# Kernel optimization log

Hardware: AMD Instinct MI355X
Metric: run time of the kernel (lower is better)

The kernel has to match this reference:

```python
import jax, jax.numpy as jnp
import numpy as np

B, S, E = 2, 2048, 1024
H = 32
DK = E // H  # 32, must equal H for the bilinear einsum to type-check
FFN = 4096
EPS = 1e-5


def layer_norm(x, g, b):
    m = jnp.mean(x, axis=-1, keepdims=True)
    v = jnp.mean((x - m) ** 2, axis=-1, keepdims=True)
    return (x - m) * jax.lax.rsqrt(v + EPS) * g + b


def setup_inputs() -> dict:
    key = jax.random.key(0)
    ks = jax.random.split(key, 16)
    sc = lambda fan_in: 1.0 / np.sqrt(fan_in)
    return {
        "x": jax.random.normal(ks[0], (B, S, E), jnp.float32),
        "Wq": jax.random.normal(ks[1], (E, E), jnp.float32) * sc(E),
        "bq": jax.random.normal(ks[2], (E,), jnp.float32) * 0.02,
        "Wk": jax.random.normal(ks[3], (E, E), jnp.float32) * sc(E),
        "bk": jax.random.normal(ks[4], (E,), jnp.float32) * 0.02,
        "Wv": jax.random.normal(ks[5], (E, E), jnp.float32) * sc(E),
        "bv": jax.random.normal(ks[6], (E,), jnp.float32) * 0.02,
        "kernelW": jax.random.normal(ks[7], (DK, H), jnp.float32),
        "Wo": jax.random.normal(ks[8], (E, E), jnp.float32) * sc(E),
        "bo": jax.random.normal(ks[9], (E,), jnp.float32) * 0.02,
        "W1": jax.random.normal(ks[10], (E, FFN), jnp.float32) * sc(E),
        "b1": jax.random.normal(ks[11], (FFN,), jnp.float32) * 0.02,
        "W2": jax.random.normal(ks[12], (FFN, E), jnp.float32) * sc(FFN),
        "b2": jax.random.normal(ks[13], (E,), jnp.float32) * 0.02,
        "g1": jnp.ones((E,), jnp.float32),
        "beta1": jnp.zeros((E,), jnp.float32),
        "g2": jnp.ones((E,), jnp.float32),
        "beta2": jnp.zeros((E,), jnp.float32),
    }


def reference(x, Wq, bq, Wk, bk, Wv, bv, kernelW, Wo, bo, W1, b1, W2, b2, g1, beta1, g2, beta2):
    # projections -> [B, H, S, DK]
    split = lambda t: t.reshape(B, S, H, DK).transpose(0, 2, 1, 3)
    q = split(x @ Wq + bq)
    k = split(x @ Wk + bk)
    v = split(x @ Wv + bv)
    # bilinear quantum-kernel score: sim[b,h,i,j] = sum_d q[b,h,i,d]*W[d,h]*k[b,h,j,d]
    sim = jnp.einsum('bhqd,dh,bhkd->bhqk', q, kernelW, k)
    attn = jax.nn.softmax(sim, axis=-1)  # dropout is identity at eval
    out = jnp.matmul(attn, v)  # [B, H, S, DK]
    out = out.transpose(0, 2, 1, 3).reshape(B, S, E) @ Wo + bo
    x = layer_norm(x + out, g1, beta1)
    ffn = jax.nn.relu(x @ W1 + b1) @ W2 + b2
    return layer_norm(x + ffn, g2, beta2)
```

## Files before the change

### kernel.cpp

```cpp
#include <hip/hip_runtime.h>


typedef unsigned short u16;
typedef unsigned int u32;
typedef __bf16 bf16x8 __attribute__((ext_vector_type(8)));
typedef float f32x4 __attribute__((ext_vector_type(4)));
typedef float f32x16 __attribute__((ext_vector_type(16)));

__device__ __forceinline__ u16 f2b(float f) {
  union { float f; unsigned u; } x; x.f = f;
  unsigned r = x.u + 0x7FFFu + ((x.u >> 16) & 1u);
  return (u16)(r >> 16);
}

__device__ __forceinline__ float b2f(u16 u) {
  union { u32 u; float f; } x; x.u = (u32)u << 16; return x.f;
}

__device__ __forceinline__ unsigned pkbf(float lo, float hi) {
  unsigned r;
  asm("v_cvt_pk_bf16_f32 %0, %1, %2" : "=v"(r) : "v"(lo), "v"(hi));
  return r;
}

__device__ __forceinline__ float expo2(float x) {
#if __has_builtin(__builtin_amdgcn_exp2f)
  return __builtin_amdgcn_exp2f(x);
#else
  return exp2f(x);
#endif
}

#define GLDS16(gp, lp)                                                         \
  __builtin_amdgcn_global_load_lds(                                            \
      (const __attribute__((address_space(1))) void*)(gp),                     \
      (__attribute__((address_space(3))) void*)(lp), 16, 0, 0)

__global__ __launch_bounds__(256) void prep_kernel(
    const float* __restrict__ Wq, const float* __restrict__ Wk,
    const float* __restrict__ Wv, const float* __restrict__ Wo,
    const float* __restrict__ W1, const float* __restrict__ W2,
    const float* __restrict__ x, u16* __restrict__ WqT, u16* __restrict__ WoT,
    u16* __restrict__ W1T, u16* __restrict__ W2T, u16* __restrict__ xb) {
  __shared__ float tile[32][33];
  const int id = blockIdx.x;
  if (id < 12288) {
    const float* W; u16* WT; int K, N, bx, by;
    if (id < 4096) {
      const int w = id >> 10, local = id & 1023;
      bx = local & 31; by = local >> 5; K = 1024; N = 1024;
      W = (w == 0) ? Wq : (w == 1) ? Wk : (w == 2) ? Wv : Wo;
      WT = (w == 0) ? WqT : (w == 1) ? WqT + 1048576
           : (w == 2) ? WqT + 2097152 : WoT;
    } else if (id < 8192) {
      const int local = id - 4096;
      bx = local & 127; by = local >> 7; K = 1024; N = 4096;
      W = W1; WT = W1T;
    } else {
      const int local = id - 8192;
      bx = local & 31; by = local >> 5; K = 4096; N = 1024;
      W = W2; WT = W2T;
    }
    const int tx = threadIdx.x & 31, ty = threadIdx.x >> 5;
    const int n0 = bx * 32, k0 = by * 32;
#pragma unroll
    for (int i = 0; i < 4; ++i)
      tile[ty + 8 * i][tx] = W[(size_t)(k0 + ty + 8 * i) * N + n0 + tx];
    __syncthreads();
#pragma unroll
    for (int i = 0; i < 4; ++i)
      WT[(size_t)(n0 + ty + 8 * i) * K + k0 + tx] = f2b(tile[tx][ty + 8 * i]);
  } else {
    const int i = (id - 12288) * 256 + threadIdx.x;
    float4 v = ((const float4*)x)[i];
    ushort4 o;
    o.x = f2b(v.x); o.y = f2b(v.y); o.z = f2b(v.z); o.w = f2b(v.w);
    ((ushort4*)xb)[i] = o;
  }
}

template <int MODE, int BN>
__global__ __launch_bounds__(256) void gemmT(
    const u16* __restrict__ A, const u16* __restrict__ BT,
    const float* __restrict__ bias, const float* __restrict__ bias2,
    const float* __restrict__ bias3, const float* __restrict__ res,
    void* __restrict__ outp, const float* __restrict__ kW, int N_, int K_) {
  constexpr int ABYT = 128 * 32 * 2;
  constexpr int BBYT = BN * 32 * 2;
  constexpr int STRIDE = ABYT + BBYT;
  constexpr int MI = (BN == 128) ? 4 : 2;
  __shared__ __align__(16) char SH[2 * STRIDE];
  const int t = threadIdx.x, lane = t & 63, wid = t >> 6;
  const int gx = gridDim.x;
  const int id = blockIdx.y * gx + blockIdx.x;
  const int nb = gx * gridDim.y;
  const int sid = (id & 7) * (nb >> 3) + (id >> 3);
  const int bx = sid % gx;
  int by = sid / gx;
  int kh6 = 0;
  if constexpr (MODE == 6 || MODE == 7) { kh6 = by >> 5; by &= 31; }
  const int m0 = by * 128, n0 = bx * BN;
  const int wr = (BN == 128) ? (wid >> 1) * 64 : wid * 32;
  const int wc = (BN == 128) ? (wid & 1) * 64 : 0;
  const int lr = lane & 15, lg = lane >> 4;
  const int K = K_;
  const int koff = (MODE == 6) ? kh6 * 1024 : (MODE == 7) ? kh6 * 512 : 0;

  f32x4 acc[MI][4] = {};

  const u16* ga0 = A + (size_t)(m0 + (t >> 2)) * K + koff + (t & 3) * 8;
  const u16* ga1 = ga0 + (size_t)64 * K;
  const u16* gb0 = BT + (size_t)(n0 + (t >> 2)) * K + koff + (t & 3) * 8;
  const u16* gb1 = gb0 + (size_t)64 * K;
  const int stA = wid * 1024;

#define STAGE(CUR, KT)                                                         \
  {                                                                            \
    char* l_ = (char*)SH + (CUR) * STRIDE + stA;                               \
    const size_t o_ = (size_t)(KT) * 32;                                       \
    GLDS16(ga0 + o_, l_);                                                      \
    GLDS16(ga1 + o_, l_ + 4096);                                               \
    GLDS16(gb0 + o_, l_ + ABYT);                                               \
    if constexpr (BN == 128) GLDS16(gb1 + o_, l_ + ABYT + 4096);               \
  }

  const int nk = (MODE == 6) ? 32 : (MODE == 7) ? 16 : (K >> 5);
  STAGE(0, 0);
  __syncthreads();
  int cur = 0;
  for (int kt = 0; kt < nk; ++kt) {
    if (kt + 1 < nk) STAGE(cur ^ 1, kt + 1);
    const char* l = (const char*)SH + cur * STRIDE;
    bf16x8 af[MI], bf[4];
#pragma unroll
    for (int i = 0; i < MI; ++i)
      af[i] = *(const bf16x8*)(l + (wr + i * 16 + lr) * 64 + lg * 16);
#pragma unroll
    for (int i = 0; i < 4; ++i)
      bf[i] = *(const bf16x8*)(l + ABYT + (wc + i * 16 + lr) * 64 + lg * 16);
#pragma unroll
    for (int mi = 0; mi < MI; ++mi)
#pragma unroll
      for (int ni = 0; ni < 4; ++ni)
        acc[mi][ni] = __builtin_amdgcn_mfma_f32_16x16x32_bf16(
            af[mi], bf[ni], acc[mi][ni], 0, 0, 0);
    __syncthreads();
    cur ^= 1;
  }
#undef STAGE

#pragma unroll
  for (int mi = 0; mi < MI; ++mi) {
#pragma unroll
    for (int ni = 0; ni < 4; ++ni) {
      const int row = m0 + wr + mi * 16 + lg * 4;
      const int col = n0 + wc + ni * 16 + lr;
      f32x4 v = acc[mi][ni];
      if constexpr (MODE == 3) {
        const float bv = bias[col];
        u16* o = (u16*)outp;
#pragma unroll
        for (int r = 0; r < 4; ++r) {
          const int rr = row + r;
          float y = v[r] + bv;
          o[(size_t)rr * N_ + col] = f2b(y > 0.f ? y : 0.f);
        }
      } else if constexpr (MODE == 6) {
        u16* o = (kh6 < 2) ? ((u16*)outp + (size_t)kh6 * 4194304)
                           : ((u16*)res + (size_t)(kh6 - 2) * 4194304);
#pragma unroll
        for (int r = 0; r < 4; ++r) {
          const int rr = row + r;
          o[(size_t)rr * N_ + col] = f2b(v[r]);
        }
      } else if constexpr (MODE == 7) {
        u16* o = (kh6 == 0) ? (u16*)outp : (u16*)res;
#pragma unroll
        for (int r = 0; r < 4; ++r) {
          const int rr = row + r;
          o[(size_t)rr * N_ + col] = f2b(v[r]);
        }
      } else {
        const int proj = col >> 10, c = col & 1023;
        const int h = c >> 5, d = c & 31;
        u16* qout = (u16*)outp;
        if (proj == 0) {
          const float bv = bias[c];
          const float sc = kW[d * 32 + h] * 1.44269504089f;
#pragma unroll
          for (int r = 0; r < 4; ++r) {
            const int rr = row + r;
            const int bb = rr >> 11, s = rr & 2047;
            qout[(size_t)(((bb * 32 + h) * 2048) + s) * 32 + d] =
                f2b((v[r] + bv) * sc);
          }
        } else if (proj == 1) {
          const float bv = bias2[c];
          u16* kout = qout + 4194304;
          const int c2 = d >> 3;
#pragma unroll
          for (int r = 0; r < 4; ++r) {
            const int rr = row + r;
            const int bb = rr >> 11, s = rr & 2047;
            const int k = s & 63;
            const int g = ((k >> 5) << 1) | (c2 >> 1);
            kout[(size_t)(bb * 32 + h) * 65536 + (s >> 6) * 2048 + g * 512 +
                 (c2 & 1) * 256 + (k & 31) * 8 + (d & 7)] = f2b(v[r] + bv);
          }
        } else {
          const float bv = bias3[c];
          u16* vout = qout + 8388608;
          const int bb = row >> 11, s0 = row & 2047;
          const int k = s0 & 63;
          const int cc = k >> 3, rb = cc >> 1, hb = cc & 1, e = k & 7;
          ushort4 st;
          st.x = f2b(v[0] + bv); st.y = f2b(v[1] + bv);
          st.z = f2b(v[2] + bv); st.w = f2b(v[3] + bv);
          *(ushort4*)(vout + (size_t)(bb * 32 + h) * 65536 +
                      (s0 >> 6) * 2048 + rb * 512 + hb * 256 + d * 8 + e) = st;
        }
      }
    }
  }
}

__device__ __forceinline__ void attn_tile(
    const bf16x8& k0, const bf16x8& k1, const bf16x8& k2, const bf16x8& k3,
    const bf16x8& v0, const bf16x8& v1, const bf16x8& v2, const bf16x8& v3,
    const bf16x8& qb0, const bf16x8& qb1,
    f32x16& acc, float& la, float& lb, float& lc, float& ld) {
  const f32x16 z16 = {};
  f32x16 s0 = __builtin_amdgcn_mfma_f32_32x32x16_bf16(k0, qb0, z16, 0, 0, 0);
  s0 = __builtin_amdgcn_mfma_f32_32x32x16_bf16(k1, qb1, s0, 0, 0, 0);
  f32x16 s1 = __builtin_amdgcn_mfma_f32_32x32x16_bf16(k2, qb0, z16, 0, 0, 0);
  s1 = __builtin_amdgcn_mfma_f32_32x32x16_bf16(k3, qb1, s1, 0, 0, 0);
  float p0[16], p1[16];
#pragma unroll
  for (int r = 0; r < 16; ++r) p0[r] = expo2(s0[r]);
#pragma unroll
  for (int r = 0; r < 16; ++r) p1[r] = expo2(s1[r]);
#pragma unroll
  for (int r = 0; r < 4; ++r) {
    la += p0[r] + p1[r];
    lb += p0[4 + r] + p1[4 + r];
    lc += p0[8 + r] + p1[8 + r];
    ld += p0[12 + r] + p1[12 + r];
  }
  {
    u32 x0 = pkbf(p0[0], p0[1]), x1 = pkbf(p0[2], p0[3]);
    u32 y0 = pkbf(p0[4], p0[5]), y1 = pkbf(p0[6], p0[7]);
    asm("v_permlane32_swap_b32 %0, %1" : "+v"(x0), "+v"(y0));
    asm("v_permlane32_swap_b32 %0, %1" : "+v"(x1), "+v"(y1));
    union { u32 d[4]; bf16x8 v; } u;
    u.d[0] = x0; u.d[1] = x1; u.d[2] = y0; u.d[3] = y1;
    acc = __builtin_amdgcn_mfma_f32_32x32x16_bf16(v0, u.v, acc, 0, 0, 0);
  }
  {
    u32 x0 = pkbf(p0[8], p0[9]), x1 = pkbf(p0[10], p0[11]);
    u32 y0 = pkbf(p0[12], p0[13]), y1 = pkbf(p0[14], p0[15]);
    asm("v_permlane32_swap_b32 %0, %1" : "+v"(x0), "+v"(y0));
    asm("v_permlane32_swap_b32 %0, %1" : "+v"(x1), "+v"(y1));
    union { u32 d[4]; bf16x8 v; } u;
    u.d[0] = x0; u.d[1] = x1; u.d[2] = y0; u.d[3] = y1;
    acc = __builtin_amdgcn_mfma_f32_32x32x16_bf16(v1, u.v, acc, 0, 0, 0);
  }
  {
    u32 x0 = pkbf(p1[0], p1[1]), x1 = pkbf(p1[2], p1[3]);
    u32 y0 = pkbf(p1[4], p1[5]), y1 = pkbf(p1[6], p1[7]);
    asm("v_permlane32_swap_b32 %0, %1" : "+v"(x0), "+v"(y0));
    asm("v_permlane32_swap_b32 %0, %1" : "+v"(x1), "+v"(y1));
    union { u32 d[4]; bf16x8 v; } u;
    u.d[0] = x0; u.d[1] = x1; u.d[2] = y0; u.d[3] = y1;
    acc = __builtin_amdgcn_mfma_f32_32x32x16_bf16(v2, u.v, acc, 0, 0, 0);
  }
  {
    u32 x0 = pkbf(p1[8], p1[9]), x1 = pkbf(p1[10], p1[11]);
    u32 y0 = pkbf(p1[12], p1[13]), y1 = pkbf(p1[14], p1[15]);
    asm("v_permlane32_swap_b32 %0, %1" : "+v"(x0), "+v"(y0));
    asm("v_permlane32_swap_b32 %0, %1" : "+v"(x1), "+v"(y1));
    union { u32 d[4]; bf16x8 v; } u;
    u.d[0] = x0; u.d[1] = x1; u.d[2] = y0; u.d[3] = y1;
    acc = __builtin_amdgcn_mfma_f32_32x32x16_bf16(v3, u.v, acc, 0, 0, 0);
  }
}

__global__ __launch_bounds__(512) void attn_kernel(
    const u16* __restrict__ Q, const u16* __restrict__ K,
    const u16* __restrict__ VT, u16* __restrict__ O) {
  __shared__ __align__(16) char LDSB[32768];
  const int t = threadIdx.x, wid = t >> 6, lane = t & 63;
  const int qg = wid & 3, kh = wid >> 2;
  const int bid = blockIdx.x;
  const int swz = (bid & 7) * 128 + (bid >> 3);
  const int bh = swz >> 4;
  const int qt = swz & 15;
  const int q0 = qt * 128 + qg * 32;
  const int lq = lane & 31, hi = lane >> 5;
  const u16* Qh = Q + (size_t)bh * 65536;
  const u16* Kh = K + (size_t)bh * 65536;
  const u16* Vh = VT + (size_t)bh * 65536;

  const bf16x8 qb0 = *(const bf16x8*)(Qh + (size_t)(q0 + lq) * 32 + hi * 8);
  const bf16x8 qb1 = *(const bf16x8*)(Qh + (size_t)(q0 + lq) * 32 + 16 + hi * 8);

  const u16* kg = Kh + wid * 512 + lane * 8;
  const u16* vg = Vh + wid * 512 + lane * 8;
  const int lds_w = wid * 1024;

#define STAGEA(CUR, I)                                                         \
  if (wid < 4) {                                                               \
    char* b_ = LDSB + (CUR) * 16384 + lds_w;                                   \
    GLDS16(kg + (size_t)(I) * 2048, b_);                                       \
    GLDS16(vg + (size_t)(I) * 2048, b_ + 4096);                                \
    GLDS16(kg + (size_t)(16 + (I)) * 2048, b_ + 8192);                         \
    GLDS16(vg + (size_t)(16 + (I)) * 2048, b_ + 12288);                        \
  }

  f32x16 acc = {};
  float la = 0.f, lb = 0.f, lc = 0.f, ld = 0.f;

  STAGEA(0, 0);
  __syncthreads();
  int cur = 0;
#pragma unroll 1
  for (int i = 0; i < 16; ++i) {
    if (i < 15) STAGEA(cur ^ 1, i + 1);
    const char* kb = LDSB + cur * 16384 + kh * 8192 + lane * 16;
    const bf16x8 ka0 = *(const bf16x8*)(kb);
    const bf16x8 ka1 = *(const bf16x8*)(kb + 1024);
    const bf16x8 ka2 = *(const bf16x8*)(kb + 2048);
    const bf16x8 ka3 = *(const bf16x8*)(kb + 3072);
    const bf16x8 va0 = *(const bf16x8*)(kb + 4096);
    const bf16x8 va1 = *(const bf16x8*)(kb + 5120);
    const bf16x8 va2 = *(const bf16x8*)(kb + 6144);
    const bf16x8 va3 = *(const bf16x8*)(kb + 7168);
    attn_tile(ka0, ka1, ka2, ka3, va0, va1, va2, va3, qb0, qb1,
              acc, la, lb, lc, ld);
    __syncthreads();
    cur ^= 1;
  }
#undef STAGEA

  float lrun = (la + lb) + (lc + ld);
  lrun += __shfl_xor(lrun, 32);

  float* sm_acc = (float*)LDSB;
  float* sm_l = (float*)(LDSB + 16384);
  if (kh == 1) {
    sm_l[qg * 32 + lq] = lrun;
#pragma unroll
    for (int r = 0; r < 16; ++r) sm_acc[(qg * 64 + lane) * 16 + r] = acc[r];
  }
  __syncthreads();
  if (kh == 0) {
    const float inv = 1.f / (lrun + sm_l[qg * 32 + lq]);
    const int bb = bh >> 5, h = bh & 31;
    u16* o = O + (size_t)(bb * 2048 + q0 + lq) * 1024 + h * 32;
#pragma unroll
    for (int g = 0; g < 4; ++g) {
      ushort4 st;
      st.x = f2b((acc[g * 4 + 0] + sm_acc[(qg * 64 + lane) * 16 + g * 4 + 0]) * inv);
      st.y = f2b((acc[g * 4 + 1] + sm_acc[(qg * 64 + lane) * 16 + g * 4 + 1]) * inv);
      st.z = f2b((acc[g * 4 + 2] + sm_acc[(qg * 64 + lane) * 16 + g * 4 + 2]) * inv);
      st.w = f2b((acc[g * 4 + 3] + sm_acc[(qg * 64 + lane) * 16 + g * 4 + 3]) * inv);
      *(ushort4*)(o + g * 8 + hi * 4) = st;
    }
  }
}

__global__ __launch_bounds__(256) void ln1merge_kernel(
    const u16* __restrict__ P0, const u16* __restrict__ P1,
    const u16* __restrict__ R, const float* __restrict__ bias,
    const float* __restrict__ g, const float* __restrict__ b,
    u16* __restrict__ out) {
  const int wid = threadIdx.x >> 6, lane = threadIdx.x & 63;
  const int row = blockIdx.x * 4 + wid;
  const ushort4* A4 = (const ushort4*)(P0 + (size_t)row * 1024);
  const ushort4* B4 = (const ushort4*)(P1 + (size_t)row * 1024);
  const ushort4* R4 = (const ushort4*)(R + (size_t)row * 1024);
  const float4* Bi4 = (const float4*)bias;
  float4 xs[4];
  float s = 0.f, sq = 0.f;
#pragma unroll
  for (int i = 0; i < 4; ++i) {
    const int c = lane + i * 64;
    const ushort4 a = A4[c], pb = B4[c], rr = R4[c];
    const float4 bi = Bi4[c];
    float4 x;
    x.x = (b2f(a.x) + b2f(pb.x)) + b2f(rr.x) + bi.x;
    x.y = (b2f(a.y) + b2f(pb.y)) + b2f(rr.y) + bi.y;
    x.z = (b2f(a.z) + b2f(pb.z)) + b2f(rr.z) + bi.z;
    x.w = (b2f(a.w) + b2f(pb.w)) + b2f(rr.w) + bi.w;
    xs[i] = x;
    s += x.x + x.y + x.z + x.w;
    sq += x.x * x.x + x.y * x.y + x.z * x.z + x.w * x.w;
  }
#pragma unroll
  for (int m = 1; m < 64; m <<= 1) { s += __shfl_xor(s, m); sq += __shfl_xor(sq, m); }
  const float mean = s * (1.f / 1024.f);
  float var = sq * (1.f / 1024.f) - mean * mean;
  var = var > 0.f ? var : 0.f;
  const float rstd = rsqrtf(var + 1e-5f);
  const float4* g4 = (const float4*)g;
  const float4* b4 = (const float4*)b;
  ushort4* of = (ushort4*)(out + (size_t)row * 1024);
#pragma unroll
  for (int i = 0; i < 4; ++i) {
    const int c = lane + i * 64;
    const float4 gv = g4[c], bv = b4[c], x = xs[i];
    ushort4 yb;
    yb.x = f2b((x.x - mean) * rstd * gv.x + bv.x);
    yb.y = f2b((x.y - mean) * rstd * gv.y + bv.y);
    yb.z = f2b((x.z - mean) * rstd * gv.z + bv.z);
    yb.w = f2b((x.w - mean) * rstd * gv.w + bv.w);
    of[c] = yb;
  }
}

__global__ __launch_bounds__(256) void ln2sum_kernel(
    const u16* __restrict__ P0, const u16* __restrict__ P1,
    const u16* __restrict__ P2, const u16* __restrict__ P3,
    const u16* __restrict__ R, const float* __restrict__ bias,
    const float* __restrict__ g, const float* __restrict__ b,
    float* __restrict__ out) {
  const int wid = threadIdx.x >> 6, lane = threadIdx.x & 63;
  const int row = blockIdx.x * 4 + wid;
  const ushort4* A4 = (const ushort4*)(P0 + (size_t)row * 1024);
  const ushort4* B4 = (const ushort4*)(P1 + (size_t)row * 1024);
  const ushort4* C4 = (const ushort4*)(P2 + (size_t)row * 1024);
  const ushort4* D4 = (const ushort4*)(P3 + (size_t)row * 1024);
  const ushort4* R4 = (const ushort4*)(R + (size_t)row * 1024);
  const float4* Bi4 = (const float4*)bias;
  float4 xs[4];
  float s = 0.f, sq = 0.f;
#pragma unroll
  for (int i = 0; i < 4; ++i) {
    const int c = lane + i * 64;
    const ushort4 a = A4[c], pb = B4[c], pc = C4[c], pd = D4[c], rr = R4[c];
    const float4 bi = Bi4[c];
    float4 x;
    x.x = (b2f(a.x) + b2f(pb.x)) + (b2f(pc.x) + b2f(pd.x)) + b2f(rr.x) + bi.x;
    x.y = (b2f(a.y) + b2f(pb.y)) + (b2f(pc.y) + b2f(pd.y)) + b2f(rr.y) + bi.y;
    x.z = (b2f(a.z) + b2f(pb.z)) + (b2f(pc.z) + b2f(pd.z)) + b2f(rr.z) + bi.z;
    x.w = (b2f(a.w) + b2f(pb.w)) + (b2f(pc.w) + b2f(pd.w)) + b2f(rr.w) + bi.w;
    xs[i] = x;
    s += x.x + x.y + x.z + x.w;
    sq += x.x * x.x + x.y * x.y + x.z * x.z + x.w * x.w;
  }
#pragma unroll
  for (int m = 1; m < 64; m <<= 1) { s += __shfl_xor(s, m); sq += __shfl_xor(sq, m); }
  const float mean = s * (1.f / 1024.f);
  float var = sq * (1.f / 1024.f) - mean * mean;
  var = var > 0.f ? var : 0.f;
  const float rstd = rsqrtf(var + 1e-5f);
  const float4* g4 = (const float4*)g;
  const float4* b4 = (const float4*)b;
  float4* of = (float4*)(out + (size_t)row * 1024);
#pragma unroll
  for (int i = 0; i < 4; ++i) {
    const int c = lane + i * 64;
    const float4 gv = g4[c], bv = b4[c], x = xs[i];
    float4 y;
    y.x = (x.x - mean) * rstd * gv.x + bv.x;
    y.y = (x.y - mean) * rstd * gv.y + bv.y;
    y.z = (x.z - mean) * rstd * gv.z + bv.z;
    y.w = (x.w - mean) * rstd * gv.w + bv.w;
    of[c] = y;
  }
}

extern "C" void kernel_launch(void* const* d_in, const int* in_sizes, int n_in,
                              void* d_out, int out_size, void* d_ws,
                              size_t ws_size, hipStream_t stream) {
  const float* x   = (const float*)d_in[0];
  const float* Wq  = (const float*)d_in[1];
  const float* bq  = (const float*)d_in[2];
  const float* Wk  = (const float*)d_in[3];
  const float* bk  = (const float*)d_in[4];
  const float* Wv  = (const float*)d_in[5];
  const float* bv  = (const float*)d_in[6];
  const float* kW  = (const float*)d_in[7];
  const float* Wo  = (const float*)d_in[8];
  const float* bo  = (const float*)d_in[9];
  const float* W1  = (const float*)d_in[10];
  const float* b1  = (const float*)d_in[11];
  const float* W2  = (const float*)d_in[12];
  const float* b2  = (const float*)d_in[13];
  const float* g1  = (const float*)d_in[14];
  const float* be1 = (const float*)d_in[15];
  const float* g2  = (const float*)d_in[16];
  const float* be2 = (const float*)d_in[17];

  char* ws = (char*)d_ws;
  const size_t MB = 1024 * 1024;
  u16*   WqT = (u16*)(ws + 0 * MB);
  u16*   WoT = (u16*)(ws + 6 * MB);
  u16*   W1T = (u16*)(ws + 8 * MB);
  u16*   W2T = (u16*)(ws + 16 * MB);
  u16*   r1b = (u16*)(ws + 24 * MB);
  u16*   xb  = (u16*)(ws + 40 * MB);
  u16*   qhB = (u16*)(ws + 48 * MB);
  u16*   khB = (u16*)(ws + 56 * MB);
  u16*   vTB = (u16*)(ws + 64 * MB);
  u16*   hf  = (u16*)(ws + 40 * MB);
  u16*   ao  = (u16*)(ws + 72 * MB);
  u16*   pw0 = (u16*)(ws + 48 * MB);
  u16*   pw1 = (u16*)(ws + 56 * MB);
  u16*   p0  = (u16*)(ws + 0 * MB);
  u16*   p2  = (u16*)(ws + 72 * MB);

  const dim3 blk(256);

  prep_kernel<<<16384, blk, 0, stream>>>(Wq, Wk, Wv, Wo, W1, W2, x,
                                         WqT, WoT, W1T, W2T, xb);

  gemmT<5, 128><<<dim3(24, 32), blk, 0, stream>>>(
      xb, WqT, bq, bk, bv, nullptr, qhB, kW, 3072, 1024);

  attn_kernel<<<1024, dim3(512), 0, stream>>>(qhB, khB, vTB, ao);

  gemmT<7, 128><<<dim3(8, 64), blk, 0, stream>>>(
      ao, WoT, nullptr, nullptr, nullptr, (const float*)pw1, pw0, nullptr,
      1024, 1024);
  ln1merge_kernel<<<1024, blk, 0, stream>>>(pw0, pw1, xb, bo, g1, be1, r1b);
  gemmT<3, 128><<<dim3(32, 32), blk, 0, stream>>>(
      r1b, W1T, b1, nullptr, nullptr, nullptr, hf, nullptr, 4096, 1024);
  gemmT<6, 128><<<dim3(8, 128), blk, 0, stream>>>(
      hf, W2T, nullptr, nullptr, nullptr, (const float*)p2, p0, nullptr,
      1024, 4096);
  ln2sum_kernel<<<1024, blk, 0, stream>>>(p0, p0 + 4194304, p2, p2 + 4194304,
                                          r1b, b2, g2, be2, (float*)d_out);

  (void)in_sizes; (void)n_in; (void)out_size; (void)ws_size;
}
```

Before: 235.9 us.

## Use 512-thread GEMM blocks with 8 waves each computing 32x64 subtiles

The GEMM kernel moves from 4 waves per 128x128 tile (64x64 per wave) to 8 waves per tile (32x64 per wave), launched with 512 threads. Each thread now stages one A and one B 16-byte chunk per K step instead of up to four, which halves per-thread accumulator registers and global-to-LDS issue. The aim is more waves in flight to hide latency. The trade-off is more LDS fragment reads relative to MFMA work and heavier barrier traffic per block.

```diff
diff --git a/kernel.cpp b/kernel.cpp
--- a/kernel.cpp
+++ b/kernel.cpp
@@ -79,16 +79,14 @@
   }
 }
 
-template <int MODE, int BN>
-__global__ __launch_bounds__(256) void gemmT(
+template <int MODE>
+__global__ __launch_bounds__(512) void gemmT(
     const u16* __restrict__ A, const u16* __restrict__ BT,
     const float* __restrict__ bias, const float* __restrict__ bias2,
     const float* __restrict__ bias3, const float* __restrict__ res,
     void* __restrict__ outp, const float* __restrict__ kW, int N_, int K_) {
   constexpr int ABYT = 128 * 32 * 2;
-  constexpr int BBYT = BN * 32 * 2;
-  constexpr int STRIDE = ABYT + BBYT;
-  constexpr int MI = (BN == 128) ? 4 : 2;
+  constexpr int STRIDE = 2 * ABYT;
   __shared__ __align__(16) char SH[2 * STRIDE];
   const int t = threadIdx.x, lane = t & 63, wid = t >> 6;
   const int gx = gridDim.x;
@@ -99,29 +97,24 @@
   int by = sid / gx;
   int kh6 = 0;
   if constexpr (MODE == 6 || MODE == 7) { kh6 = by >> 5; by &= 31; }
-  const int m0 = by * 128, n0 = bx * BN;
-  const int wr = (BN == 128) ? (wid >> 1) * 64 : wid * 32;
-  const int wc = (BN == 128) ? (wid & 1) * 64 : 0;
+  const int m0 = by * 128, n0 = bx * 128;
+  const int wr = (wid >> 1) * 32, wc = (wid & 1) * 64;
   const int lr = lane & 15, lg = lane >> 4;
   const int K = K_;
   const int koff = (MODE == 6) ? kh6 * 1024 : (MODE == 7) ? kh6 * 512 : 0;
 
-  f32x4 acc[MI][4] = {};
+  f32x4 acc[2][4] = {};
 
   const u16* ga0 = A + (size_t)(m0 + (t >> 2)) * K + koff + (t & 3) * 8;
-  const u16* ga1 = ga0 + (size_t)64 * K;
   const u16* gb0 = BT + (size_t)(n0 + (t >> 2)) * K + koff + (t & 3) * 8;
-  const u16* gb1 = gb0 + (size_t)64 * K;
-  const int stA = wid * 1024;
+  const int st16 = t * 16;
 
 #define STAGE(CUR, KT)                                                         \
   {                                                                            \
-    char* l_ = (char*)SH + (CUR) * STRIDE + stA;                               \
+    char* l_ = (char*)SH + (CUR) * STRIDE + st16;                              \
     const size_t o_ = (size_t)(KT) * 32;                                       \
     GLDS16(ga0 + o_, l_);                                                      \
-    GLDS16(ga1 + o_, l_ + 4096);                                               \
     GLDS16(gb0 + o_, l_ + ABYT);                                               \
-    if constexpr (BN == 128) GLDS16(gb1 + o_, l_ + ABYT + 4096);               \
   }
 
   const int nk = (MODE == 6) ? 32 : (MODE == 7) ? 16 : (K >> 5);
@@ -131,15 +124,15 @@
   for (int kt = 0; kt < nk; ++kt) {
     if (kt + 1 < nk) STAGE(cur ^ 1, kt + 1);
     const char* l = (const char*)SH + cur * STRIDE;
-    bf16x8 af[MI], bf[4];
-#pragma unroll
-    for (int i = 0; i < MI; ++i)
+    bf16x8 af[2], bf[4];
+#pragma unroll
+    for (int i = 0; i < 2; ++i)
       af[i] = *(const bf16x8*)(l + (wr + i * 16 + lr) * 64 + lg * 16);
 #pragma unroll
     for (int i = 0; i < 4; ++i)
       bf[i] = *(const bf16x8*)(l + ABYT + (wc + i * 16 + lr) * 64 + lg * 16);
 #pragma unroll
-    for (int mi = 0; mi < MI; ++mi)
+    for (int mi = 0; mi < 2; ++mi)
 #pragma unroll
       for (int ni = 0; ni < 4; ++ni)
         acc[mi][ni] = __builtin_amdgcn_mfma_f32_16x16x32_bf16(
@@ -150,7 +143,7 @@
 #undef STAGE
 
 #pragma unroll
-  for (int mi = 0; mi < MI; ++mi) {
+  for (int mi = 0; mi < 2; ++mi) {
 #pragma unroll
     for (int ni = 0; ni < 4; ++ni) {
       const int row = m0 + wr + mi * 16 + lg * 4;
@@ -510,22 +503,23 @@
   u16*   p2  = (u16*)(ws + 72 * MB);
 
   const dim3 blk(256);
+  const dim3 blkG(512);
 
   prep_kernel<<<16384, blk, 0, stream>>>(Wq, Wk, Wv, Wo, W1, W2, x,
                                          WqT, WoT, W1T, W2T, xb);
 
-  gemmT<5, 128><<<dim3(24, 32), blk, 0, stream>>>(
+  gemmT<5><<<dim3(24, 32), blkG, 0, stream>>>(
       xb, WqT, bq, bk, bv, nullptr, qhB, kW, 3072, 1024);
 
-  attn_kernel<<<1024, dim3(512), 0, stream>>>(qhB, khB, vTB, ao);
-
-  gemmT<7, 128><<<dim3(8, 64), blk, 0, stream>>>(
+  attn_kernel<<<1024, blkG, 0, stream>>>(qhB, khB, vTB, ao);
+
+  gemmT<7><<<dim3(8, 64), blkG, 0, stream>>>(
       ao, WoT, nullptr, nullptr, nullptr, (const float*)pw1, pw0, nullptr,
       1024, 1024);
   ln1merge_kernel<<<1024, blk, 0, stream>>>(pw0, pw1, xb, bo, g1, be1, r1b);
-  gemmT<3, 128><<<dim3(32, 32), blk, 0, stream>>>(
+  gemmT<3><<<dim3(32, 32), blkG, 0, stream>>>(
       r1b, W1T, b1, nullptr, nullptr, nullptr, hf, nullptr, 4096, 1024);
-  gemmT<6, 128><<<dim3(8, 128), blk, 0, stream>>>(
+  gemmT<6><<<dim3(8, 128), blkG, 0, stream>>>(
       hf, W2T, nullptr, nullptr, nullptr, (const float*)p2, p0, nullptr,
       1024, 4096);
   ln2sum_kernel<<<1024, blk, 0, stream>>>(p0, p0 + 4194304, p2, p2 + 4194304,
```

New measurement: 236.2 us. Within noise of the previous version (+0.1%).
